# Kernel tuning notes

Hardware: AMD Instinct MI355X
Metric: run time of the kernel (lower is better)

## Reference

```python
import jax, jax.numpy as jnp
import numpy as np

VOCAB = 256
D_MODEL = 1792
NUM_LAYERS = 4
D_STATE = 16
D_CONV = 4
EXPAND = 2
D_INNER = EXPAND * D_MODEL            # 3584
DT_RANK = (D_MODEL + 15) // 16        # 112
EPS = 1e-5


def _ln(x, w, b):
    x32 = x.astype(jnp.float32)
    mu = x32.mean(-1, keepdims=True)
    var = ((x32 - mu) ** 2).mean(-1, keepdims=True)
    return (((x32 - mu) * jax.lax.rsqrt(var + EPS)) * w + b)


def _silu(x):
    return x * jax.nn.sigmoid(x)


def _mamba_mixer(x, in_w, cw, cb, xp_w, dt_w, dt_b, A_log, Dp, out_w):
    # x: [B, L, d_model]
    B, L, _ = x.shape
    xz = jnp.einsum('bld,ed->ble', x, in_w)          # [B, L, 2*d_inner]
    xc, z = jnp.split(xz, 2, axis=-1)
    # depthwise causal conv1d over time
    xc = jax.lax.conv_general_dilated(
        xc.swapaxes(1, 2), cw[:, None, :], (1,), [(D_CONV - 1, 0)],
        feature_group_count=D_INNER,
        dimension_numbers=('NCH', 'OIH', 'NCH')).swapaxes(1, 2) + cb
    xc = _silu(xc)
    dbl = jnp.einsum('bld,ed->ble', xc, xp_w)        # [B, L, dt_rank+2*d_state]
    dt = dbl[..., :DT_RANK]
    Bm = dbl[..., DT_RANK:DT_RANK + D_STATE]
    Cm = dbl[..., DT_RANK + D_STATE:]
    dt = jax.nn.softplus(jnp.einsum('blr,dr->bld', dt, dt_w) + dt_b)  # [B,L,d_inner]
    A = -jnp.exp(A_log)                              # [d_inner, d_state]
    dA = jnp.exp(dt[..., None] * A)                  # [B, L, d_inner, d_state]
    dBx = dt[..., None] * Bm[:, :, None, :] * xc[..., None]

    def step(h, t):
        dA_t, dBx_t, C_t = t
        h = dA_t * h + dBx_t                         # [B, d_inner, d_state]
        y = jnp.einsum('bds,bs->bd', h, C_t)
        return h, y

    h0 = jnp.zeros((B, D_INNER, D_STATE), x.dtype)
    _, ys = jax.lax.scan(step, h0, (dA.swapaxes(0, 1), dBx.swapaxes(0, 1), Cm.swapaxes(0, 1)))
    y = ys.swapaxes(0, 1) + Dp * xc                  # [B, L, d_inner]
    y = y * _silu(z)
    return jnp.einsum('bld,od->blo', y, out_w)       # [B, L, d_model]


def setup_inputs() -> dict:
    key = jax.random.key(0)
    ks = jax.random.split(key, 10)
    B, L = 1, 512
    s = 0.02
    input_ids = jax.random.randint(ks[0], (B, L), 0, VOCAB, dtype=jnp.int32)
    embed = jax.random.normal(ks[1], (VOCAB, D_MODEL), jnp.float32) * s
    in_proj_w = jax.random.normal(ks[2], (NUM_LAYERS, 2 * D_INNER, D_MODEL), jnp.float32) * s
    conv_w = jax.random.normal(ks[3], (NUM_LAYERS, D_INNER, D_CONV), jnp.float32) * 0.1
    conv_b = jnp.zeros((NUM_LAYERS, D_INNER), jnp.float32)
    x_proj_w = jax.random.normal(ks[4], (NUM_LAYERS, DT_RANK + 2 * D_STATE, D_INNER), jnp.float32) * s
    dt_proj_w = jax.random.normal(ks[5], (NUM_LAYERS, D_INNER, DT_RANK), jnp.float32) * (DT_RANK ** -0.5)
    u = jax.random.uniform(ks[6], (NUM_LAYERS, D_INNER), jnp.float32)
    dt = jnp.exp(u * (jnp.log(0.1) - jnp.log(0.001)) + jnp.log(0.001))
    dt_proj_b = dt + jnp.log(-jnp.expm1(-dt))        # inverse softplus
    A_log = jnp.log(jnp.broadcast_to(jnp.arange(1, D_STATE + 1, dtype=jnp.float32), (NUM_LAYERS, D_INNER, D_STATE))) + jnp.zeros((NUM_LAYERS, D_INNER, D_STATE), jnp.float32)
    D_skip = jnp.ones((NUM_LAYERS, D_INNER), jnp.float32)
    out_proj_w = jax.random.normal(ks[7], (NUM_LAYERS, D_MODEL, D_INNER), jnp.float32) * s
    norm_w = jnp.ones((NUM_LAYERS, D_MODEL), jnp.float32)
    norm_b = jnp.zeros((NUM_LAYERS, D_MODEL), jnp.float32)
    final_norm_w = jnp.ones((D_MODEL,), jnp.float32)
    final_norm_b = jnp.zeros((D_MODEL,), jnp.float32)
    return dict(input_ids=input_ids, embed=embed, in_proj_w=in_proj_w, conv_w=conv_w,
                conv_b=conv_b, x_proj_w=x_proj_w, dt_proj_w=dt_proj_w, dt_proj_b=dt_proj_b,
                A_log=A_log, D_skip=D_skip, out_proj_w=out_proj_w, norm_w=norm_w,
                norm_b=norm_b, final_norm_w=final_norm_w, final_norm_b=final_norm_b)


def reference(input_ids, embed, in_proj_w, conv_w, conv_b, x_proj_w, dt_proj_w,
              dt_proj_b, A_log, D_skip, out_proj_w, norm_w, norm_b,
              final_norm_w, final_norm_b):
    hidden = embed[input_ids]                        # [B, L, d_model]
    residual = hidden.astype(jnp.float32)            # residual_in_fp32
    for i in range(NUM_LAYERS):
        if i > 0:
            residual = residual + hidden.astype(jnp.float32)
        h = _ln(residual, norm_w[i], norm_b[i])
        hidden = _mamba_mixer(h, in_proj_w[i], conv_w[i], conv_b[i], x_proj_w[i],
                              dt_proj_w[i], dt_proj_b[i], A_log[i], D_skip[i], out_proj_w[i])
    residual = residual + hidden.astype(jnp.float32)
    return _ln(residual, final_norm_w, final_norm_b)
```

## Files before the change

kernel.cpp:

```cpp
#include <hip/hip_runtime.h>
#include <hip/hip_bf16.h>
#include <math.h>

#define D_MODEL 1792
#define D_INNER 3584
#define D_STATE 16
#define D_CONV  4
#define DT_RANK 112
#define NLAYER  4
#define LSEQ    512
#define XPROJ_N (DT_RANK + 2 * D_STATE)
#define KSPLIT  8
#define KCHUNK  (D_INNER / KSPLIT)
#define SCH     32
#define SCL     (LSEQ / SCH)
#define INSPLIT 2
#define OUTSPLIT 4

typedef __attribute__((ext_vector_type(8))) short bf16x8;
typedef __attribute__((ext_vector_type(8))) ushort u16x8;
typedef __attribute__((ext_vector_type(4))) ushort u16x4;
typedef __attribute__((ext_vector_type(4))) float f32x4;

__device__ __forceinline__ ushort f2bf(float f) {
    unsigned u = __float_as_uint(f);
    unsigned r = (u + 0x7FFFu + ((u >> 16) & 1u)) >> 16;
    return (ushort)r;
}

__global__ __launch_bounds__(256) void wcvt_all(const float* __restrict__ in_w,
                                                const float* __restrict__ out_w,
                                                const float* __restrict__ x_w,
                                                const float* __restrict__ dt_w,
                                                ushort* __restrict__ inb,
                                                ushort* __restrict__ outb,
                                                ushort* __restrict__ xb,
                                                ushort* __restrict__ dtwb) {
    const int n8_in  = NLAYER * 2 * D_INNER * D_MODEL / 8;
    const int n8_out = NLAYER * D_MODEL * D_INNER / 8;
    const int n8_x   = NLAYER * XPROJ_N * D_INNER / 8;
    const int n8_dt  = NLAYER * D_INNER * 128 / 8;
    int idx = blockIdx.x * 256 + threadIdx.x;

    const float* src; ushort* dst; int j;
    if (idx < n8_in)                          { src = in_w;  dst = inb;  j = idx; }
    else if (idx < n8_in + n8_out)            { src = out_w; dst = outb; j = idx - n8_in; }
    else if (idx < n8_in + n8_out + n8_x)     { src = x_w;   dst = xb;   j = idx - n8_in - n8_out; }
    else if (idx < n8_in + n8_out + n8_x + n8_dt) {
        j = idx - n8_in - n8_out - n8_x;
        int col8 = j & 15;
        int row  = j >> 4;
        u16x8 v = {};
        if (col8 < DT_RANK / 8) {
            const float* p = dt_w + (size_t)row * DT_RANK + col8 * 8;
            const f32x4 a = *(const f32x4*)p;
            const f32x4 b = *(const f32x4*)(p + 4);
            v[0] = f2bf(a[0]); v[1] = f2bf(a[1]); v[2] = f2bf(a[2]); v[3] = f2bf(a[3]);
            v[4] = f2bf(b[0]); v[5] = f2bf(b[1]); v[6] = f2bf(b[2]); v[7] = f2bf(b[3]);
        }
        *(u16x8*)(dtwb + (size_t)j * 8) = v;
        return;
    } else return;

    const f32x4 a = *((const f32x4*)src + (size_t)j * 2);
    const f32x4 b = *((const f32x4*)src + (size_t)j * 2 + 1);
    u16x8 v;
    v[0] = f2bf(a[0]); v[1] = f2bf(a[1]); v[2] = f2bf(a[2]); v[3] = f2bf(a[3]);
    v[4] = f2bf(b[0]); v[5] = f2bf(b[1]); v[6] = f2bf(b[2]); v[7] = f2bf(b[3]);
    *(u16x8*)(dst + (size_t)j * 8) = v;
}

__global__ __launch_bounds__(256) void add_ln_kernel(float* __restrict__ res,
                                                     const float* __restrict__ hidp,
                                                     const float* __restrict__ w,
                                                     const float* __restrict__ b,
                                                     float* __restrict__ out32,
                                                     ushort* __restrict__ out16,
                                                     int mode,
                                                     const int* __restrict__ ids,
                                                     const float* __restrict__ embed) {
    const int l = blockIdx.x;
    const int t = threadIdx.x;
    __shared__ float sbuf[8];
    float loc[7];
    float* row = res + (size_t)l * D_MODEL;
    const float* erow = (mode == 2) ? (embed + (size_t)ids[l] * D_MODEL) : nullptr;

    float sum = 0.f;
#pragma unroll
    for (int i = 0; i < 7; ++i) {
        int d = t + i * 256;
        float v;
        if (mode == 2) {
            v = erow[d]; row[d] = v;
        } else {
            v = row[d];
            if (mode == 1) {
                float hv = 0.f;
#pragma unroll
                for (int z = 0; z < OUTSPLIT; ++z)
                    hv += hidp[(size_t)z * LSEQ * D_MODEL + (size_t)l * D_MODEL + d];
                v += hv; row[d] = v;
            }
        }
        loc[i] = v;
        sum += v;
    }
#pragma unroll
    for (int o = 32; o > 0; o >>= 1) sum += __shfl_down(sum, o, 64);
    if ((t & 63) == 0) sbuf[t >> 6] = sum;
    __syncthreads();
    if (t == 0) sbuf[4] = sbuf[0] + sbuf[1] + sbuf[2] + sbuf[3];
    __syncthreads();
    const float mu = sbuf[4] * (1.f / D_MODEL);

    float vs = 0.f;
#pragma unroll
    for (int i = 0; i < 7; ++i) { float d0 = loc[i] - mu; vs += d0 * d0; }
#pragma unroll
    for (int o = 32; o > 0; o >>= 1) vs += __shfl_down(vs, o, 64);
    __syncthreads();
    if ((t & 63) == 0) sbuf[t >> 6] = vs;
    __syncthreads();
    if (t == 0) sbuf[4] = sbuf[0] + sbuf[1] + sbuf[2] + sbuf[3];
    __syncthreads();
    const float rstd = rsqrtf(sbuf[4] * (1.f / D_MODEL) + 1e-5f);

#pragma unroll
    for (int i = 0; i < 7; ++i) {
        int d = t + i * 256;
        float v = (loc[i] - mu) * rstd * w[d] + b[d];
        if (out16) out16[(size_t)l * D_MODEL + d] = f2bf(v);
        else       out32[(size_t)l * D_MODEL + d] = v;
    }
}

template<int NSPLIT>
__global__ __launch_bounds__(256) void gemm128_mfma(const ushort* __restrict__ A, int lda,
                                                    const ushort* __restrict__ W,
                                                    float* __restrict__ C,
                                                    int N, int K) {
    constexpr int BK = 32;
    __shared__ ushort As[128 * BK];
    __shared__ ushort Bs[128 * BK];

    const int tid  = threadIdx.x;
    const int lane = tid & 63;
    const int wave = tid >> 6;
    const int m0 = blockIdx.y * 128;
    const int n0 = blockIdx.x * 128;
    const int wm = (wave >> 1) * 64;
    const int wn = (wave & 1) * 64;
    const int frow = lane & 15;
    const int fkg  = lane >> 4;
    const int kchunk = K / NSPLIT;
    const int kbase  = blockIdx.z * kchunk;
    const int M = gridDim.y * 128;

    f32x4 acc[4][4] = {};

    for (int it = 0; it < kchunk / BK; ++it) {
        const int k0 = kbase + it * BK;
#pragma unroll
        for (int i = 0; i < 2; ++i) {
            int c = tid + i * 256;
            int row = c >> 2;
            int kc  = (c & 3) * 8;
            __builtin_amdgcn_global_load_lds(
                (const __attribute__((address_space(1))) void*)(A + (size_t)(m0 + row) * lda + k0 + kc),
                (__attribute__((address_space(3))) void*)(As + c * 8), 16, 0, 0);
        }
#pragma unroll
        for (int i = 0; i < 2; ++i) {
            int c = tid + i * 256;
            int row = c >> 2;
            int kc  = (c & 3) * 8;
            __builtin_amdgcn_global_load_lds(
                (const __attribute__((address_space(1))) void*)(W + (size_t)(n0 + row) * K + k0 + kc),
                (__attribute__((address_space(3))) void*)(Bs + c * 8), 16, 0, 0);
        }
        __syncthreads();

        bf16x8 af[4];
#pragma unroll
        for (int i = 0; i < 4; ++i)
            af[i] = *(const bf16x8*)(As + (wm + i * 16 + frow) * BK + fkg * 8);

#pragma unroll
        for (int j = 0; j < 4; ++j) {
            bf16x8 bb = *(const bf16x8*)(Bs + (wn + j * 16 + frow) * BK + fkg * 8);
#pragma unroll
            for (int i = 0; i < 4; ++i)
                acc[i][j] = __builtin_amdgcn_mfma_f32_16x16x32_bf16(af[i], bb, acc[i][j], 0, 0, 0);
        }
        __syncthreads();
    }

    float* Cz = C + (size_t)blockIdx.z * M * N;
#pragma unroll
    for (int i = 0; i < 4; ++i) {
#pragma unroll
        for (int r = 0; r < 4; ++r) {
            int m = m0 + wm + i * 16 + fkg * 4 + r;
            float* cp = Cz + (size_t)m * N + n0 + wn + frow;
#pragma unroll
            for (int j = 0; j < 4; ++j)
                cp[j * 16] = acc[i][j][r];
        }
    }
}

template<int ACT, int NSPLIT>
__global__ __launch_bounds__(256) void gemm_mfma(const ushort* __restrict__ A, int lda,
                                                 const ushort* __restrict__ W,
                                                 float* __restrict__ C,
                                                 int N, int K,
                                                 const float* __restrict__ bias) {
    constexpr int BM = 64;
    constexpr int BK = 32;
    __shared__ ushort As[BM * BK];
    __shared__ ushort Bs[128 * BK];

    const int tid  = threadIdx.x;
    const int lane = tid & 63;
    const int wave = tid >> 6;
    const int m0 = blockIdx.y * BM;
    const int n0 = blockIdx.x * 128;
    const int wm = (wave >> 1) * 32;
    const int wn = (wave & 1) * 64;
    const int frow = lane & 15;
    const int fkg  = lane >> 4;
    const int kchunk = K / NSPLIT;
    const int kbase  = blockIdx.z * kchunk;
    const int M = gridDim.y * BM;

    f32x4 acc[2][4] = {};

    for (int it = 0; it < kchunk / BK; ++it) {
        const int k0 = kbase + it * BK;
        {
            int row = tid >> 2;
            int kc  = (tid & 3) * 8;
            __builtin_amdgcn_global_load_lds(
                (const __attribute__((address_space(1))) void*)(A + (size_t)(m0 + row) * lda + k0 + kc),
                (__attribute__((address_space(3))) void*)(As + tid * 8), 16, 0, 0);
        }
#pragma unroll
        for (int i = 0; i < 2; ++i) {
            int c = tid + i * 256;
            int row = c >> 2;
            int kc  = (c & 3) * 8;
            __builtin_amdgcn_global_load_lds(
                (const __attribute__((address_space(1))) void*)(W + (size_t)(n0 + row) * K + k0 + kc),
                (__attribute__((address_space(3))) void*)(Bs + c * 8), 16, 0, 0);
        }
        __syncthreads();

        bf16x8 af[2];
#pragma unroll
        for (int i = 0; i < 2; ++i)
            af[i] = *(const bf16x8*)(As + (wm + i * 16 + frow) * BK + fkg * 8);

#pragma unroll
        for (int j = 0; j < 4; ++j) {
            bf16x8 bb = *(const bf16x8*)(Bs + (wn + j * 16 + frow) * BK + fkg * 8);
#pragma unroll
            for (int i = 0; i < 2; ++i)
                acc[i][j] = __builtin_amdgcn_mfma_f32_16x16x32_bf16(af[i], bb, acc[i][j], 0, 0, 0);
        }
        __syncthreads();
    }

    float bj[4];
    if (ACT) {
#pragma unroll
        for (int j = 0; j < 4; ++j) bj[j] = bias[n0 + wn + frow + j * 16];
    }

    float* Cz = C + (size_t)blockIdx.z * M * N;
#pragma unroll
    for (int i = 0; i < 2; ++i) {
#pragma unroll
        for (int r = 0; r < 4; ++r) {
            int m = m0 + wm + i * 16 + fkg * 4 + r;
            float* cp = Cz + (size_t)m * N + n0 + wn + frow;
#pragma unroll
            for (int j = 0; j < 4; ++j) {
                float v = acc[i][j][r];
                if (ACT) {
                    v += bj[j];
                    v = (v > 20.f) ? v : __logf(1.f + __expf(v));
                }
                cp[j * 16] = v;
            }
        }
    }
}

__global__ __launch_bounds__(256) void xproj_split(const ushort* __restrict__ xcbf,
                                                   const ushort* __restrict__ W,
                                                   float* __restrict__ xpart) {
    __shared__ ushort As[64 * 32];
    __shared__ ushort Ws[16 * 32];
    const int tid  = threadIdx.x;
    const int lane = tid & 63;
    const int wave = tid >> 6;
    const int n0 = blockIdx.x * 16;
    const int m0 = blockIdx.y * 64;
    const int z  = blockIdx.z;
    const int wm = wave * 16;
    const int frow = lane & 15;
    const int fkg  = lane >> 4;
    const int kbase = z * KCHUNK;

    f32x4 acc = {};

    for (int it = 0; it < KCHUNK / 32; ++it) {
        const int k0 = kbase + it * 32;
        {
            int row = tid >> 2;
            int kc  = (tid & 3) * 8;
            __builtin_amdgcn_global_load_lds(
                (const __attribute__((address_space(1))) void*)(xcbf + (size_t)(m0 + row) * D_INNER + k0 + kc),
                (__attribute__((address_space(3))) void*)(As + tid * 8), 16, 0, 0);
        }
        if (tid < 64) {
            int row = tid >> 2;
            int kc  = (tid & 3) * 8;
            __builtin_amdgcn_global_load_lds(
                (const __attribute__((address_space(1))) void*)(W + (size_t)(n0 + row) * D_INNER + k0 + kc),
                (__attribute__((address_space(3))) void*)(Ws + tid * 8), 16, 0, 0);
        }
        __syncthreads();

        bf16x8 af = *(const bf16x8*)(As + (wm + frow) * 32 + fkg * 8);
        bf16x8 bb = *(const bf16x8*)(Ws + frow * 32 + fkg * 8);
        acc = __builtin_amdgcn_mfma_f32_16x16x32_bf16(af, bb, acc, 0, 0, 0);
        __syncthreads();
    }

#pragma unroll
    for (int r = 0; r < 4; ++r) {
        int m = m0 + wm + fkg * 4 + r;
        int n = n0 + frow;
        xpart[((size_t)z * LSEQ + m) * XPROJ_N + n] = acc[r];
    }
}

__global__ __launch_bounds__(256) void xreduce_kernel(const float* __restrict__ xpart,
                                                      float* __restrict__ dbl,
                                                      ushort* __restrict__ dtb) {
    int idx = blockIdx.x * 256 + threadIdx.x;
    if (idx >= LSEQ * XPROJ_N) return;
    int m = idx / XPROJ_N;
    int n = idx - m * XPROJ_N;
    float s = 0.f;
#pragma unroll
    for (int z = 0; z < KSPLIT; ++z)
        s += xpart[(size_t)z * LSEQ * XPROJ_N + idx];
    dbl[idx] = s;
    if (n < DT_RANK)      dtb[m * 128 + n] = f2bf(s);
    else if (n < 128)     dtb[m * 128 + n] = 0;
}

__global__ __launch_bounds__(256) void conv_silu_kernel(const float* __restrict__ xzp,
                                                        const float* __restrict__ cw,
                                                        const float* __restrict__ cb,
                                                        float* __restrict__ xc,
                                                        ushort* __restrict__ xcbf) {
    const size_t SL = (size_t)LSEQ * 2 * D_INNER;
    int idx = blockIdx.x * 256 + threadIdx.x;
    if (idx >= LSEQ * D_INNER / 4) return;
    int l  = idx / (D_INNER / 4);
    int c4 = (idx - l * (D_INNER / 4)) * 4;

    const f32x4 wc0 = *(const f32x4*)(cw + (size_t)(c4 + 0) * D_CONV);
    const f32x4 wc1 = *(const f32x4*)(cw + (size_t)(c4 + 1) * D_CONV);
    const f32x4 wc2 = *(const f32x4*)(cw + (size_t)(c4 + 2) * D_CONV);
    const f32x4 wc3 = *(const f32x4*)(cw + (size_t)(c4 + 3) * D_CONV);

    f32x4 s = *(const f32x4*)(cb + c4);
#pragma unroll
    for (int k = 0; k < D_CONV; ++k) {
        int ll = l - (D_CONV - 1) + k;
        if (ll >= 0) {
            const f32x4 v0 = *(const f32x4*)(xzp + (size_t)ll * (2 * D_INNER) + c4);
            const f32x4 v1 = *(const f32x4*)(xzp + SL + (size_t)ll * (2 * D_INNER) + c4);
            s[0] = fmaf(wc0[k], v0[0] + v1[0], s[0]);
            s[1] = fmaf(wc1[k], v0[1] + v1[1], s[1]);
            s[2] = fmaf(wc2[k], v0[2] + v1[2], s[2]);
            s[3] = fmaf(wc3[k], v0[3] + v1[3], s[3]);
        }
    }
    f32x4 o;
    u16x4 ob;
#pragma unroll
    for (int q = 0; q < 4; ++q) {
        const float sig = 1.f / (1.f + __expf(-s[q]));
        o[q] = s[q] * sig;
        ob[q] = f2bf(o[q]);
    }
    *(f32x4*)(xc + (size_t)idx * 4) = o;
    *(u16x4*)(xcbf + (size_t)idx * 4) = ob;
}

__global__ __launch_bounds__(256) void scan_part1(const float* __restrict__ dt,
                                                  const float* __restrict__ xc,
                                                  const float* __restrict__ dbl,
                                                  const float* __restrict__ A_log,
                                                  float* __restrict__ P,
                                                  float* __restrict__ F) {
    const int d = blockIdx.x * 256 + threadIdx.x;
    const int c = blockIdx.y;
    __shared__ float Bs[SCL][D_STATE];
    {
        int t = threadIdx.x;
        int ll = t >> 4, s = t & 15;
        Bs[ll][s] = dbl[(size_t)(c * SCL + ll) * XPROJ_N + DT_RANK + s];
    }
    float A2[D_STATE], h[D_STATE], p[D_STATE];
#pragma unroll
    for (int s = 0; s < D_STATE; ++s) {
        A2[s] = -__expf(A_log[(size_t)d * D_STATE + s]) * 1.4426950408889634f;
        h[s] = 0.f; p[s] = 1.f;
    }
    __syncthreads();

    for (int li0 = 0; li0 < SCL; li0 += 4) {
        float dtv4[4], xcv4[4];
#pragma unroll
        for (int q = 0; q < 4; ++q) {
            const int l = c * SCL + li0 + q;
            dtv4[q] = dt[(size_t)l * D_INNER + d];
            xcv4[q] = xc[(size_t)l * D_INNER + d];
        }
#pragma unroll
        for (int q = 0; q < 4; ++q) {
            const int li = li0 + q;
            const float dtv = dtv4[q];
            const float coef = dtv * xcv4[q];
#pragma unroll
            for (int s = 0; s < D_STATE; ++s) {
                float e = exp2f(dtv * A2[s]);
                h[s] = fmaf(e, h[s], coef * Bs[li][s]);
                p[s] *= e;
            }
        }
    }
    float* Pp = P + ((size_t)c * D_INNER + d) * D_STATE;
    float* Fp = F + ((size_t)c * D_INNER + d) * D_STATE;
#pragma unroll
    for (int v = 0; v < 4; ++v) {
        *(f32x4*)(Pp + v * 4) = *(f32x4*)(p + v * 4);
        *(f32x4*)(Fp + v * 4) = *(f32x4*)(h + v * 4);
    }
}

__global__ __launch_bounds__(256) void scan_fix(const float* __restrict__ P,
                                                const float* __restrict__ F,
                                                float* __restrict__ Hin) {
    const int idx = blockIdx.x * 256 + threadIdx.x;
    if (idx >= D_INNER * D_STATE) return;
    const size_t stride = (size_t)D_INNER * D_STATE;
    float h = 0.f;
#pragma unroll
    for (int c = 0; c < SCH; ++c) {
        Hin[c * stride + idx] = h;
        h = fmaf(P[c * stride + idx], h, F[c * stride + idx]);
    }
}

__global__ __launch_bounds__(256) void scan_part3(const float* __restrict__ dt,
                                                  const float* __restrict__ xc,
                                                  const float* __restrict__ dbl,
                                                  const float* __restrict__ A_log,
                                                  const float* __restrict__ Dp,
                                                  const float* __restrict__ xzp,
                                                  const float* __restrict__ Hin,
                                                  ushort* __restrict__ ybf) {
    const size_t SL = (size_t)LSEQ * 2 * D_INNER;
    const int d = blockIdx.x * 256 + threadIdx.x;
    const int c = blockIdx.y;
    __shared__ float Bs[SCL][D_STATE];
    __shared__ float Cs[SCL][D_STATE];
    {
        int t = threadIdx.x;
        int ll = t >> 4, s = t & 15;
        Bs[ll][s] = dbl[(size_t)(c * SCL + ll) * XPROJ_N + DT_RANK + s];
        Cs[ll][s] = dbl[(size_t)(c * SCL + ll) * XPROJ_N + DT_RANK + D_STATE + s];
    }
    float A2[D_STATE], h[D_STATE];
#pragma unroll
    for (int s = 0; s < D_STATE; ++s)
        A2[s] = -__expf(A_log[(size_t)d * D_STATE + s]) * 1.4426950408889634f;
    {
        const float* Hp = Hin + ((size_t)c * D_INNER + d) * D_STATE;
#pragma unroll
        for (int v = 0; v < 4; ++v)
            *(f32x4*)(h + v * 4) = *(const f32x4*)(Hp + v * 4);
    }
    const float Dd = Dp[d];
    __syncthreads();

    for (int li0 = 0; li0 < SCL; li0 += 4) {
        float dtv4[4], xcv4[4], zv4[4];
#pragma unroll
        for (int q = 0; q < 4; ++q) {
            const int l = c * SCL + li0 + q;
            dtv4[q] = dt[(size_t)l * D_INNER + d];
            xcv4[q] = xc[(size_t)l * D_INNER + d];
            zv4[q]  = xzp[(size_t)l * (2 * D_INNER) + D_INNER + d]
                    + xzp[SL + (size_t)l * (2 * D_INNER) + D_INNER + d];
        }
#pragma unroll
        for (int q = 0; q < 4; ++q) {
            const int li = li0 + q;
            const float dtv = dtv4[q];
            const float xcv = xcv4[q];
            const float coef = dtv * xcv;
            float a0 = 0.f, a1 = 0.f, a2 = 0.f, a3 = 0.f;
#pragma unroll
            for (int s = 0; s < D_STATE; s += 4) {
                float e0 = exp2f(dtv * A2[s + 0]);
                float e1 = exp2f(dtv * A2[s + 1]);
                float e2 = exp2f(dtv * A2[s + 2]);
                float e3 = exp2f(dtv * A2[s + 3]);
                h[s + 0] = fmaf(e0, h[s + 0], coef * Bs[li][s + 0]);
                h[s + 1] = fmaf(e1, h[s + 1], coef * Bs[li][s + 1]);
                h[s + 2] = fmaf(e2, h[s + 2], coef * Bs[li][s + 2]);
                h[s + 3] = fmaf(e3, h[s + 3], coef * Bs[li][s + 3]);
                a0 = fmaf(h[s + 0], Cs[li][s + 0], a0);
                a1 = fmaf(h[s + 1], Cs[li][s + 1], a1);
                a2 = fmaf(h[s + 2], Cs[li][s + 2], a2);
                a3 = fmaf(h[s + 3], Cs[li][s + 3], a3);
            }
            const float zv = zv4[q];
            const float sig = 1.f / (1.f + __expf(-zv));
            const float y = ((a0 + a1) + (a2 + a3) + Dd * xcv) * (zv * sig);
            ybf[(size_t)(c * SCL + li) * D_INNER + d] = f2bf(y);
        }
    }
}

extern "C" void kernel_launch(void* const* d_in, const int* in_sizes, int n_in,
                              void* d_out, int out_size, void* d_ws, size_t ws_size,
                              hipStream_t stream) {
    const int*   ids       = (const int*)d_in[0];
    const float* embed     = (const float*)d_in[1];
    const float* in_proj_w = (const float*)d_in[2];
    const float* conv_w    = (const float*)d_in[3];
    const float* conv_b    = (const float*)d_in[4];
    const float* x_proj_w  = (const float*)d_in[5];
    const float* dt_proj_w = (const float*)d_in[6];
    const float* dt_proj_b = (const float*)d_in[7];
    const float* A_log     = (const float*)d_in[8];
    const float* D_skip    = (const float*)d_in[9];
    const float* out_proj_w= (const float*)d_in[10];
    const float* norm_w    = (const float*)d_in[11];
    const float* norm_b    = (const float*)d_in[12];
    const float* fin_w     = (const float*)d_in[13];
    const float* fin_b     = (const float*)d_in[14];
    float* out = (float*)d_out;

    float* ws = (float*)d_ws;
    float* res    = ws; ws += LSEQ * D_MODEL;
    float* xzp    = ws; ws += (size_t)INSPLIT * LSEQ * 2 * D_INNER;
    float* xc     = ws; ws += (size_t)LSEQ * D_INNER;
    float* dbl    = ws; ws += LSEQ * XPROJ_N;
    float* dty    = ws; ws += (size_t)LSEQ * D_INNER;
    float* xpart  = ws; ws += (size_t)KSPLIT * LSEQ * XPROJ_N;
    float* Pbuf   = ws; ws += (size_t)SCH * D_INNER * D_STATE;
    float* Fbuf   = ws; ws += (size_t)SCH * D_INNER * D_STATE;
    float* HinB   = ws; ws += (size_t)SCH * D_INNER * D_STATE;
    ushort* hbf   = (ushort*)ws; ws += (LSEQ * D_MODEL) / 2;
    ushort* ybf   = (ushort*)ws; ws += (LSEQ * D_INNER) / 2;
    ushort* xcbf  = (ushort*)ws; ws += (LSEQ * D_INNER) / 2;
    ushort* dtb   = (ushort*)ws; ws += (LSEQ * 128) / 2;
    ushort* inw_bf  = (ushort*)ws; ws += (size_t)NLAYER * 2 * D_INNER * D_MODEL / 2;
    ushort* outw_bf = (ushort*)ws; ws += (size_t)NLAYER * D_MODEL * D_INNER / 2;
    ushort* xw_bf   = (ushort*)ws; ws += (size_t)NLAYER * XPROJ_N * D_INNER / 2;
    ushort* dtw_bf  = (ushort*)ws; ws += (size_t)NLAYER * D_INNER * 128 / 2;
    float* outp = Pbuf;

    {
        const int n8_total = NLAYER * (2 * D_INNER * D_MODEL + D_MODEL * D_INNER
                                       + XPROJ_N * D_INNER + D_INNER * 128) / 8;
        wcvt_all<<<(n8_total + 255) / 256, 256, 0, stream>>>(
            in_proj_w, out_proj_w, x_proj_w, dt_proj_w,
            inw_bf, outw_bf, xw_bf, dtw_bf);
    }

    for (int i = 0; i < NLAYER; ++i) {
        add_ln_kernel<<<LSEQ, 256, 0, stream>>>(
            res, outp, norm_w + (size_t)i * D_MODEL, norm_b + (size_t)i * D_MODEL,
            nullptr, hbf, i > 0 ? 1 : 2, ids, embed);

        gemm128_mfma<INSPLIT><<<dim3(2 * D_INNER / 128, LSEQ / 128, INSPLIT), 256, 0, stream>>>(
            hbf, D_MODEL, inw_bf + (size_t)i * 2 * D_INNER * D_MODEL, xzp,
            2 * D_INNER, D_MODEL);

        conv_silu_kernel<<<(LSEQ * D_INNER / 4 + 255) / 256, 256, 0, stream>>>(
            xzp, conv_w + (size_t)i * D_INNER * D_CONV, conv_b + (size_t)i * D_INNER,
            xc, xcbf);

        xproj_split<<<dim3(XPROJ_N / 16, LSEQ / 64, KSPLIT), 256, 0, stream>>>(
            xcbf, xw_bf + (size_t)i * XPROJ_N * D_INNER, xpart);
        xreduce_kernel<<<(LSEQ * XPROJ_N + 255) / 256, 256, 0, stream>>>(xpart, dbl, dtb);

        gemm_mfma<1, 1><<<dim3(D_INNER / 128, LSEQ / 64, 1), 256, 0, stream>>>(
            dtb, 128, dtw_bf + (size_t)i * D_INNER * 128, dty,
            D_INNER, 128, dt_proj_b + (size_t)i * D_INNER);

        scan_part1<<<dim3(D_INNER / 256, SCH), 256, 0, stream>>>(
            dty, xc, dbl, A_log + (size_t)i * D_INNER * D_STATE, Pbuf, Fbuf);
        scan_fix<<<(D_INNER * D_STATE + 255) / 256, 256, 0, stream>>>(Pbuf, Fbuf, HinB);
        scan_part3<<<dim3(D_INNER / 256, SCH), 256, 0, stream>>>(
            dty, xc, dbl, A_log + (size_t)i * D_INNER * D_STATE,
            D_skip + (size_t)i * D_INNER, xzp, HinB, ybf);

        gemm128_mfma<OUTSPLIT><<<dim3(D_MODEL / 128, LSEQ / 128, OUTSPLIT), 256, 0, stream>>>(
            ybf, D_INNER, outw_bf + (size_t)i * D_MODEL * D_INNER, outp,
            D_MODEL, D_INNER);
    }

    add_ln_kernel<<<LSEQ, 256, 0, stream>>>(res, outp, fin_w, fin_b, out, nullptr, 1,
                                            nullptr, nullptr);
}
```

Before: 995.6 us.

## Fuse fp32-to-bf16 weight conversion into GEMM tile loads, drop conversion pass

Removes the separate kernel that converted every layer's projection weights to bf16 in a workspace. The in-proj, out-proj, x-proj and dt-proj GEMMs now load fp32 weights directly and convert them to bf16 in registers before writing to LDS. This removes a full read-and-write pass over all weights plus the later bf16 re-read. In exchange, each GEMM tile reads twice as many weight bytes, repeated across M blocks, and gives up the async global_load_lds path for the B operand.

```diff
diff --git a/kernel.cpp b/kernel.cpp
--- a/kernel.cpp
+++ b/kernel.cpp
@@ -28,46 +28,11 @@
     return (ushort)r;
 }
 
-__global__ __launch_bounds__(256) void wcvt_all(const float* __restrict__ in_w,
-                                                const float* __restrict__ out_w,
-                                                const float* __restrict__ x_w,
-                                                const float* __restrict__ dt_w,
-                                                ushort* __restrict__ inb,
-                                                ushort* __restrict__ outb,
-                                                ushort* __restrict__ xb,
-                                                ushort* __restrict__ dtwb) {
-    const int n8_in  = NLAYER * 2 * D_INNER * D_MODEL / 8;
-    const int n8_out = NLAYER * D_MODEL * D_INNER / 8;
-    const int n8_x   = NLAYER * XPROJ_N * D_INNER / 8;
-    const int n8_dt  = NLAYER * D_INNER * 128 / 8;
-    int idx = blockIdx.x * 256 + threadIdx.x;
-
-    const float* src; ushort* dst; int j;
-    if (idx < n8_in)                          { src = in_w;  dst = inb;  j = idx; }
-    else if (idx < n8_in + n8_out)            { src = out_w; dst = outb; j = idx - n8_in; }
-    else if (idx < n8_in + n8_out + n8_x)     { src = x_w;   dst = xb;   j = idx - n8_in - n8_out; }
-    else if (idx < n8_in + n8_out + n8_x + n8_dt) {
-        j = idx - n8_in - n8_out - n8_x;
-        int col8 = j & 15;
-        int row  = j >> 4;
-        u16x8 v = {};
-        if (col8 < DT_RANK / 8) {
-            const float* p = dt_w + (size_t)row * DT_RANK + col8 * 8;
-            const f32x4 a = *(const f32x4*)p;
-            const f32x4 b = *(const f32x4*)(p + 4);
-            v[0] = f2bf(a[0]); v[1] = f2bf(a[1]); v[2] = f2bf(a[2]); v[3] = f2bf(a[3]);
-            v[4] = f2bf(b[0]); v[5] = f2bf(b[1]); v[6] = f2bf(b[2]); v[7] = f2bf(b[3]);
-        }
-        *(u16x8*)(dtwb + (size_t)j * 8) = v;
-        return;
-    } else return;
-
-    const f32x4 a = *((const f32x4*)src + (size_t)j * 2);
-    const f32x4 b = *((const f32x4*)src + (size_t)j * 2 + 1);
+__device__ __forceinline__ u16x8 cvt8(const f32x4 a, const f32x4 b) {
     u16x8 v;
     v[0] = f2bf(a[0]); v[1] = f2bf(a[1]); v[2] = f2bf(a[2]); v[3] = f2bf(a[3]);
     v[4] = f2bf(b[0]); v[5] = f2bf(b[1]); v[6] = f2bf(b[2]); v[7] = f2bf(b[3]);
-    *(u16x8*)(dst + (size_t)j * 8) = v;
+    return v;
 }
 
 __global__ __launch_bounds__(256) void add_ln_kernel(float* __restrict__ res,
@@ -137,7 +102,7 @@
 
 template<int NSPLIT>
 __global__ __launch_bounds__(256) void gemm128_mfma(const ushort* __restrict__ A, int lda,
-                                                    const ushort* __restrict__ W,
+                                                    const float* __restrict__ W,
                                                     float* __restrict__ C,
                                                     int N, int K) {
     constexpr int BK = 32;
@@ -170,14 +135,20 @@
                 (const __attribute__((address_space(1))) void*)(A + (size_t)(m0 + row) * lda + k0 + kc),
                 (__attribute__((address_space(3))) void*)(As + c * 8), 16, 0, 0);
         }
+        f32x4 w0[2], w1[2];
 #pragma unroll
         for (int i = 0; i < 2; ++i) {
             int c = tid + i * 256;
             int row = c >> 2;
             int kc  = (c & 3) * 8;
-            __builtin_amdgcn_global_load_lds(
-                (const __attribute__((address_space(1))) void*)(W + (size_t)(n0 + row) * K + k0 + kc),
-                (__attribute__((address_space(3))) void*)(Bs + c * 8), 16, 0, 0);
+            const float* p = W + (size_t)(n0 + row) * K + k0 + kc;
+            w0[i] = *(const f32x4*)p;
+            w1[i] = *(const f32x4*)(p + 4);
+        }
+#pragma unroll
+        for (int i = 0; i < 2; ++i) {
+            int c = tid + i * 256;
+            *(u16x8*)(Bs + c * 8) = cvt8(w0[i], w1[i]);
         }
         __syncthreads();
 
@@ -210,14 +181,13 @@
     }
 }
 
-template<int ACT, int NSPLIT>
-__global__ __launch_bounds__(256) void gemm_mfma(const ushort* __restrict__ A, int lda,
-                                                 const ushort* __restrict__ W,
-                                                 float* __restrict__ C,
-                                                 int N, int K,
-                                                 const float* __restrict__ bias) {
+__global__ __launch_bounds__(256) void dt_gemm(const ushort* __restrict__ A,
+                                               const float* __restrict__ Wdt,
+                                               float* __restrict__ C,
+                                               const float* __restrict__ bias) {
     constexpr int BM = 64;
     constexpr int BK = 32;
+    constexpr int N = D_INNER;
     __shared__ ushort As[BM * BK];
     __shared__ ushort Bs[128 * BK];
 
@@ -230,29 +200,36 @@
     const int wn = (wave & 1) * 64;
     const int frow = lane & 15;
     const int fkg  = lane >> 4;
-    const int kchunk = K / NSPLIT;
-    const int kbase  = blockIdx.z * kchunk;
-    const int M = gridDim.y * BM;
 
     f32x4 acc[2][4] = {};
 
-    for (int it = 0; it < kchunk / BK; ++it) {
-        const int k0 = kbase + it * BK;
+    for (int it = 0; it < 128 / BK; ++it) {
+        const int k0 = it * BK;
         {
             int row = tid >> 2;
             int kc  = (tid & 3) * 8;
             __builtin_amdgcn_global_load_lds(
-                (const __attribute__((address_space(1))) void*)(A + (size_t)(m0 + row) * lda + k0 + kc),
+                (const __attribute__((address_space(1))) void*)(A + (size_t)(m0 + row) * 128 + k0 + kc),
                 (__attribute__((address_space(3))) void*)(As + tid * 8), 16, 0, 0);
         }
+        f32x4 w0[2], w1[2];
+        int valid[2];
 #pragma unroll
         for (int i = 0; i < 2; ++i) {
             int c = tid + i * 256;
             int row = c >> 2;
-            int kc  = (c & 3) * 8;
-            __builtin_amdgcn_global_load_lds(
-                (const __attribute__((address_space(1))) void*)(W + (size_t)(n0 + row) * K + k0 + kc),
-                (__attribute__((address_space(3))) void*)(Bs + c * 8), 16, 0, 0);
+            int k   = k0 + (c & 3) * 8;
+            valid[i] = (k < DT_RANK);
+            const float* p = Wdt + (size_t)(n0 + row) * DT_RANK + (valid[i] ? k : 0);
+            w0[i] = *(const f32x4*)p;
+            w1[i] = *(const f32x4*)(p + 4);
+        }
+#pragma unroll
+        for (int i = 0; i < 2; ++i) {
+            int c = tid + i * 256;
+            u16x8 v = {};
+            if (valid[i]) v = cvt8(w0[i], w1[i]);
+            *(u16x8*)(Bs + c * 8) = v;
         }
         __syncthreads();
 
@@ -272,25 +249,19 @@
     }
 
     float bj[4];
-    if (ACT) {
-#pragma unroll
-        for (int j = 0; j < 4; ++j) bj[j] = bias[n0 + wn + frow + j * 16];
-    }
-
-    float* Cz = C + (size_t)blockIdx.z * M * N;
+#pragma unroll
+    for (int j = 0; j < 4; ++j) bj[j] = bias[n0 + wn + frow + j * 16];
+
 #pragma unroll
     for (int i = 0; i < 2; ++i) {
 #pragma unroll
         for (int r = 0; r < 4; ++r) {
             int m = m0 + wm + i * 16 + fkg * 4 + r;
-            float* cp = Cz + (size_t)m * N + n0 + wn + frow;
+            float* cp = C + (size_t)m * N + n0 + wn + frow;
 #pragma unroll
             for (int j = 0; j < 4; ++j) {
-                float v = acc[i][j][r];
-                if (ACT) {
-                    v += bj[j];
-                    v = (v > 20.f) ? v : __logf(1.f + __expf(v));
-                }
+                float v = acc[i][j][r] + bj[j];
+                v = (v > 20.f) ? v : __logf(1.f + __expf(v));
                 cp[j * 16] = v;
             }
         }
@@ -298,7 +269,7 @@
 }
 
 __global__ __launch_bounds__(256) void xproj_split(const ushort* __restrict__ xcbf,
-                                                   const ushort* __restrict__ W,
+                                                   const float* __restrict__ W,
                                                    float* __restrict__ xpart) {
     __shared__ ushort As[64 * 32];
     __shared__ ushort Ws[16 * 32];
@@ -327,9 +298,10 @@
         if (tid < 64) {
             int row = tid >> 2;
             int kc  = (tid & 3) * 8;
-            __builtin_amdgcn_global_load_lds(
-                (const __attribute__((address_space(1))) void*)(W + (size_t)(n0 + row) * D_INNER + k0 + kc),
-                (__attribute__((address_space(3))) void*)(Ws + tid * 8), 16, 0, 0);
+            const float* p = W + (size_t)(n0 + row) * D_INNER + k0 + kc;
+            f32x4 a = *(const f32x4*)p;
+            f32x4 b = *(const f32x4*)(p + 4);
+            *(u16x8*)(Ws + tid * 8) = cvt8(a, b);
         }
         __syncthreads();
 
@@ -576,19 +548,7 @@
     ushort* ybf   = (ushort*)ws; ws += (LSEQ * D_INNER) / 2;
     ushort* xcbf  = (ushort*)ws; ws += (LSEQ * D_INNER) / 2;
     ushort* dtb   = (ushort*)ws; ws += (LSEQ * 128) / 2;
-    ushort* inw_bf  = (ushort*)ws; ws += (size_t)NLAYER * 2 * D_INNER * D_MODEL / 2;
-    ushort* outw_bf = (ushort*)ws; ws += (size_t)NLAYER * D_MODEL * D_INNER / 2;
-    ushort* xw_bf   = (ushort*)ws; ws += (size_t)NLAYER * XPROJ_N * D_INNER / 2;
-    ushort* dtw_bf  = (ushort*)ws; ws += (size_t)NLAYER * D_INNER * 128 / 2;
     float* outp = Pbuf;
-
-    {
-        const int n8_total = NLAYER * (2 * D_INNER * D_MODEL + D_MODEL * D_INNER
-                                       + XPROJ_N * D_INNER + D_INNER * 128) / 8;
-        wcvt_all<<<(n8_total + 255) / 256, 256, 0, stream>>>(
-            in_proj_w, out_proj_w, x_proj_w, dt_proj_w,
-            inw_bf, outw_bf, xw_bf, dtw_bf);
-    }
 
     for (int i = 0; i < NLAYER; ++i) {
         add_ln_kernel<<<LSEQ, 256, 0, stream>>>(
@@ -596,7 +556,7 @@
             nullptr, hbf, i > 0 ? 1 : 2, ids, embed);
 
         gemm128_mfma<INSPLIT><<<dim3(2 * D_INNER / 128, LSEQ / 128, INSPLIT), 256, 0, stream>>>(
-            hbf, D_MODEL, inw_bf + (size_t)i * 2 * D_INNER * D_MODEL, xzp,
+            hbf, D_MODEL, in_proj_w + (size_t)i * 2 * D_INNER * D_MODEL, xzp,
             2 * D_INNER, D_MODEL);
 
         conv_silu_kernel<<<(LSEQ * D_INNER / 4 + 255) / 256, 256, 0, stream>>>(
@@ -604,12 +564,12 @@
             xc, xcbf);
 
         xproj_split<<<dim3(XPROJ_N / 16, LSEQ / 64, KSPLIT), 256, 0, stream>>>(
-            xcbf, xw_bf + (size_t)i * XPROJ_N * D_INNER, xpart);
+            xcbf, x_proj_w + (size_t)i * XPROJ_N * D_INNER, xpart);
         xreduce_kernel<<<(LSEQ * XPROJ_N + 255) / 256, 256, 0, stream>>>(xpart, dbl, dtb);
 
-        gemm_mfma<1, 1><<<dim3(D_INNER / 128, LSEQ / 64, 1), 256, 0, stream>>>(
-            dtb, 128, dtw_bf + (size_t)i * D_INNER * 128, dty,
-            D_INNER, 128, dt_proj_b + (size_t)i * D_INNER);
+        dt_gemm<<<dim3(D_INNER / 128, LSEQ / 64, 1), 256, 0, stream>>>(
+            dtb, dt_proj_w + (size_t)i * D_INNER * DT_RANK, dty,
+            dt_proj_b + (size_t)i * D_INNER);
 
         scan_part1<<<dim3(D_INNER / 256, SCH), 256, 0, stream>>>(
             dty, xc, dbl, A_log + (size_t)i * D_INNER * D_STATE, Pbuf, Fbuf);
@@ -619,7 +579,7 @@
             D_skip + (size_t)i * D_INNER, xzp, HinB, ybf);
 
         gemm128_mfma<OUTSPLIT><<<dim3(D_MODEL / 128, LSEQ / 128, OUTSPLIT), 256, 0, stream>>>(
-            ybf, D_INNER, outw_bf + (size_t)i * D_MODEL * D_INNER, outp,
+            ybf, D_INNER, out_proj_w + (size_t)i * D_MODEL * D_INNER, outp,
             D_MODEL, D_INNER);
     }
 
```

After: 1.007 ms. About the same (+1.2%).
